# Optimization experiments

Hardware: AMD Instinct MI355X
Metric: run time of the kernel (lower is better)

The kernel has to match this reference:

```python
import jax, jax.numpy as jnp
import numpy as np

MARGIN = 1.0
EPS = 1e-6  # torch.nn.PairwiseDistance default eps (added to the difference vector)


def setup_inputs() -> dict:
    key = jax.random.key(0)
    k1, k2 = jax.random.split(key)
    B, D = 8192, 256
    out = jax.random.normal(k1, (B, D), dtype=jnp.float32)
    label = jax.random.randint(k2, (B,), 0, 2, dtype=jnp.int64)
    return {"out": out, "label": label}


def reference(out, label):
    B, D = out.shape
    # PairwiseDistance: dist_ij = || out_i - out_j + eps ||_2
    # Expand: sum_k (d_k + eps)^2 = ||d||^2 + 2*eps*sum_k d_k + D*eps^2
    sq_norm = jnp.sum(out * out, axis=-1)                       # [B]
    gram = out @ out.T                                          # [B, B]
    sq = sq_norm[:, None] + sq_norm[None, :] - 2.0 * gram       # ||out_i - out_j||^2
    row_sum = jnp.sum(out, axis=-1)                             # [B]
    sq_eps = sq + 2.0 * EPS * (row_sum[:, None] - row_sum[None, :]) + D * EPS * EPS
    dist = jnp.sqrt(jnp.maximum(sq_eps, 1e-12))                 # [B, B]

    same = label[:, None] == label[None, :]                     # [B, B] bool
    pos = dist * dist
    neg = jnp.square(jnp.maximum(MARGIN - dist, 0.0))
    per_pair = jnp.where(same, pos, neg)

    # only i < j pairs (strict upper triangle)
    tri = jnp.triu(jnp.ones((B, B), dtype=out.dtype), k=1)
    loss = jnp.sum(per_pair * tri)
    cnt = B * (B - 1) // 2
    return loss / (cnt + 1e-6)
```

## Files before the change

kernel.cpp:

```cpp
#include <hip/hip_runtime.h>
#include <hip/hip_fp8.h>

#define B_ 8192
#define D_ 256
#define KS_ 64
#define EPS_ 1e-6f
#define MARGIN_ 1.0f
#define NT_ 64
#define NTILES_ (NT_ * (NT_ + 1) / 2)
#define CEPS_ ((float)D_ * EPS_ * EPS_)
#define SCREEN_ 17.0f

typedef float floatx4 __attribute__((ext_vector_type(4)));

#define XBF_BYTES (B_ * D_ * 2)
#define OFF_P    0
#define OFF_Q    8192
#define OFF_S0   16384
#define OFF_S1   16640
#define OFF_N0   16896
#define OFF_N1   16897
#define OFF_C0   16898
#define OFF_ACC  16899
#define OFF_CNT  16900

__device__ __forceinline__ int trif(int t) { return (t * (129 - t)) / 2; }
__device__ __forceinline__ int decode_ti(int t) {
    int ti = (int)((129.0f - sqrtf(fmaxf(16641.0f - 8.0f * (float)t, 0.0f))) * 0.5f);
    ti = max(0, min(63, ti));
    while (trif(ti + 1) <= t) ++ti;
    while (trif(ti) > t) --ti;
    return ti;
}

__device__ __noinline__ float exact_hinge(const float* __restrict__ x, int gi, int gj,
                                          const int* __restrict__ label) {
    if (label[gi] == label[gj]) return 0.0f;
    const float* xi = x + (size_t)gi * D_;
    const float* xj = x + (size_t)gj * D_;
    float sq = 0.0f;
    for (int k = 0; k < D_; ++k) {
        const float df = xi[k] - xj[k] + EPS_;
        sq += df * df;
    }
    if (sq < 1.0f) {
        const float d = sqrtf(fmaxf(sq, 1e-12f));
        const float h = MARGIN_ - d;
        return h * h;
    }
    return 0.0f;
}

__global__ __launch_bounds__(256) void prep_kernel(
    const float* __restrict__ x, const int* __restrict__ label,
    unsigned char* __restrict__ xqT, float* __restrict__ fws) {
    float* pS = fws + OFF_P;   float* qS = fws + OFF_Q;

    __shared__ int lab_s[32];
    __shared__ float spn[32];
    __shared__ float colbuf0[4][256], colbuf1[4][256];

    const int blk = blockIdx.x;
    const int r0 = blk * 32;
    const int tid = threadIdx.x, w = tid >> 6, lane = tid & 63;

    if (blk == 0 && tid == 0) *(unsigned int*)(fws + OFF_CNT) = 0u;

    if (tid < 32) lab_s[tid] = label[r0 + tid];
    __syncthreads();

    floatx4 t0 = (floatx4)0.0f, t1 = (floatx4)0.0f;
    #pragma unroll
    for (int i = 0; i < 8; ++i) {
        const int rloc = w * 8 + i;
        const int row = r0 + rloc;
        const floatx4 v = *(const floatx4*)(x + (size_t)row * D_ + lane * 4);
        float sq = v[0]*v[0] + v[1]*v[1] + v[2]*v[2] + v[3]*v[3];
        float rs = v[0] + v[1] + v[2] + v[3];
        #pragma unroll
        for (int off = 8; off; off >>= 1) {
            sq += __shfl_down(sq, off);
            rs += __shfl_down(rs, off);
        }
        const float sqS = sq, rsS = rs;
        sq += __shfl_down(sq, 16); rs += __shfl_down(rs, 16);
        sq += __shfl_down(sq, 32); rs += __shfl_down(rs, 32);
        if (lane == 0) {
            pS[row] = sqS + 2.0f * EPS_ * rsS;
            qS[row] = sqS - 2.0f * EPS_ * rsS;
            spn[rloc] = sq;
        }
        if (lab_s[rloc]) t1 += v; else t0 += v;
        if (lane < 16) {
            __hip_fp8_e4m3 c0(v[0]), c1(v[1]), c2(v[2]), c3(v[3]);
            const unsigned int u = (unsigned int)c0.__x | ((unsigned int)c1.__x << 8)
                                 | ((unsigned int)c2.__x << 16) | ((unsigned int)c3.__x << 24);
            const int R = row >> 4, r = row & 15;
            const int ks = lane >> 3, quad = (lane >> 1) & 3, b = (lane & 1) * 4;
            *(unsigned int*)(xqT + (((R * 2 + ks) << 9) | (quad << 7) | (r << 3) | b)) = u;
        }
    }
    *(floatx4*)&colbuf0[w][lane * 4] = t0;
    *(floatx4*)&colbuf1[w][lane * 4] = t1;
    __syncthreads();

    atomicAdd(fws + OFF_S0 + tid,
              colbuf0[0][tid] + colbuf0[1][tid] + colbuf0[2][tid] + colbuf0[3][tid]);
    atomicAdd(fws + OFF_S1 + tid,
              colbuf1[0][tid] + colbuf1[1][tid] + colbuf1[2][tid] + colbuf1[3][tid]);

    if (tid < 32) {
        const float n = spn[tid];
        const int lb = lab_s[tid];
        float n0 = lb ? 0.0f : n, n1 = lb ? n : 0.0f;
        float c0 = lb ? 0.0f : 1.0f;
        #pragma unroll
        for (int off = 16; off; off >>= 1) {
            n0 += __shfl_down(n0, off);
            n1 += __shfl_down(n1, off);
            c0 += __shfl_down(c0, off);
        }
        if (tid == 0) {
            atomicAdd(fws + OFF_N0, n0);
            atomicAdd(fws + OFF_N1, n1);
            atomicAdd(fws + OFF_C0, c0);
        }
    }
}

__global__ __launch_bounds__(256, 3) void detect_kernel(
    const unsigned char* __restrict__ xqT, const float* __restrict__ x,
    const int* __restrict__ label, float* __restrict__ fws,
    float* __restrict__ out) {
    const float* pS = fws + OFF_P;  const float* qS = fws + OFF_Q;
    float* acc = fws + OFF_ACC;

    __shared__ int is_last;
    __shared__ float red[4];

    const int ti = decode_ti(blockIdx.x);
    const int tj = ti + (blockIdx.x - trif(ti));
    const int i0 = ti * 128, j0 = tj * 128;

    const int tid = threadIdx.x, wave = tid >> 6, lane = tid & 63;
    const int quad = lane >> 4, r = lane & 15;
    const int wm = wave >> 1, wn = wave & 1;

    const int Ri = (i0 >> 4) + wm * 4;
    const int Rj = (j0 >> 4) + wn * 4;
    const int lo = (quad << 7) | (r << 3);
    long av[8], bv[8];
    #pragma unroll
    for (int mt = 0; mt < 4; ++mt)
        #pragma unroll
        for (int ks = 0; ks < 2; ++ks) {
            av[mt * 2 + ks] = *(const long*)(xqT + ((((Ri + mt) * 2 + ks) << 9) | lo));
            bv[mt * 2 + ks] = *(const long*)(xqT + ((((Rj + mt) * 2 + ks) << 9) | lo));
        }

    floatx4 accv[16];
    #pragma unroll
    for (int t = 0; t < 16; ++t) accv[t] = (floatx4)0.0f;

    #pragma unroll
    for (int ks = 0; ks < 2; ++ks)
        #pragma unroll
        for (int mt = 0; mt < 4; ++mt)
            #pragma unroll
            for (int nt = 0; nt < 4; ++nt)
                accv[mt * 4 + nt] = __builtin_amdgcn_mfma_f32_16x16x32_fp8_fp8(
                    av[mt * 2 + ks], bv[nt * 2 + ks], accv[mt * 4 + nt], 0, 0, 0);

    float s = 0.0f;
    if (ti != tj) {
        float m = -1e30f;
        #pragma unroll
        for (int t = 0; t < 16; ++t)
            m = fmaxf(m, fmaxf(fmaxf(accv[t][0], accv[t][1]), fmaxf(accv[t][2], accv[t][3])));
        float pv = pS[i0 + wm * 64 + lane];
        float qv = qS[j0 + wn * 64 + lane];
        #pragma unroll
        for (int off = 32; off; off >>= 1) {
            pv = fminf(pv, __shfl_down(pv, off));
            qv = fminf(qv, __shfl_down(qv, off));
        }
        const float pmn = __shfl(pv, 0), qmn = __shfl(qv, 0);
        if (__any(2.0f * m > pmn + qmn - SCREEN_)) {
            float psr[16], qsr[4];
            #pragma unroll
            for (int mt = 0; mt < 4; ++mt)
                #pragma unroll
                for (int reg = 0; reg < 4; ++reg)
                    psr[mt * 4 + reg] = pS[i0 + wm * 64 + mt * 16 + quad * 4 + reg];
            #pragma unroll
            for (int nt = 0; nt < 4; ++nt)
                qsr[nt] = qS[j0 + wn * 64 + nt * 16 + r];
            #pragma unroll
            for (int mt = 0; mt < 4; ++mt)
                #pragma unroll
                for (int nt = 0; nt < 4; ++nt)
                    #pragma unroll
                    for (int reg = 0; reg < 4; ++reg) {
                        const float sq8 = psr[mt * 4 + reg] + qsr[nt]
                                        - 2.0f * accv[mt * 4 + nt][reg];
                        if (sq8 < SCREEN_) {
                            const int gi = i0 + wm * 64 + mt * 16 + quad * 4 + reg;
                            const int gj = j0 + wn * 64 + nt * 16 + r;
                            s += exact_hinge(x, gi, gj, label);
                        }
                    }
        }
    } else {
        float psr[16], qsr[4];
        #pragma unroll
        for (int mt = 0; mt < 4; ++mt)
            #pragma unroll
            for (int reg = 0; reg < 4; ++reg)
                psr[mt * 4 + reg] = pS[i0 + wm * 64 + mt * 16 + quad * 4 + reg];
        #pragma unroll
        for (int nt = 0; nt < 4; ++nt)
            qsr[nt] = qS[j0 + wn * 64 + nt * 16 + r];
        #pragma unroll
        for (int mt = 0; mt < 4; ++mt)
            #pragma unroll
            for (int nt = 0; nt < 4; ++nt)
                #pragma unroll
                for (int reg = 0; reg < 4; ++reg) {
                    const int il = wm * 64 + mt * 16 + quad * 4 + reg;
                    const int jl = wn * 64 + nt * 16 + r;
                    if (il < jl) {
                        const float sq8 = psr[mt * 4 + reg] + qsr[nt]
                                        - 2.0f * accv[mt * 4 + nt][reg];
                        if (sq8 < SCREEN_)
                            s += exact_hinge(x, i0 + il, j0 + jl, label);
                    }
                }
    }
    #pragma unroll
    for (int off = 32; off; off >>= 1) s += __shfl_down(s, off);
    if (lane == 0 && s != 0.0f) atomicAdd(acc, s);

    asm volatile("s_waitcnt vmcnt(0)" ::: "memory");
    __syncthreads();
    if (tid == 0) {
        const unsigned int old = atomicAdd((unsigned int*)(fws + OFF_CNT), 1u);
        is_last = (old == (unsigned int)(NTILES_ - 1));
    }
    __syncthreads();
    if (!is_last) return;

    const float a = fws[OFF_S0 + tid], b = fws[OFF_S1 + tid];
    float v = a * a + b * b;
    #pragma unroll
    for (int off = 32; off; off >>= 1) v += __shfl_down(v, off);
    if (lane == 0) red[wave] = v;
    __syncthreads();

    if (tid == 0) {
        const double Tsq = (double)red[0] + (double)red[1] + (double)red[2] + (double)red[3];
        const double N0 = fws[OFF_N0], N1 = fws[OFF_N1];
        const double C0r = fws[OFF_C0];
        const double C0 = (double)(long long)(C0r + 0.5);
        const double C1 = (double)B_ - C0;
        const double same = C0 * N0 + C1 * N1 - Tsq
                          + 0.5 * (C0 * (C0 - 1.0) + C1 * (C1 - 1.0)) * (double)CEPS_;
        const float hinge = atomicAdd(acc, 0.0f);
        const double total = same + (double)hinge;
        const double cnt = (double)B_ * (double)(B_ - 1) / 2.0 + 1e-6;
        out[0] = (float)(total / cnt);
    }
}

extern "C" void kernel_launch(void* const* d_in, const int* in_sizes, int n_in,
                              void* d_out, int out_size, void* d_ws, size_t ws_size,
                              hipStream_t stream) {
    const float* x = (const float*)d_in[0];
    const int* label = (const int*)d_in[1];
    float* out = (float*)d_out;

    char* ws = (char*)d_ws;
    unsigned char* xqT = (unsigned char*)ws;
    float* fws = (float*)(ws + XBF_BYTES);

    prep_kernel<<<B_ / 32, 256, 0, stream>>>(x, label, xqT, fws);
    detect_kernel<<<NTILES_, 256, 0, stream>>>(xqT, x, label, fws, out);
}
```

Baseline: 100.4 us.

## Process four column tiles per detect block and widen prep blocks

Each detect block now walks a chunk of up to four column tiles for one row tile. It reuses the A-fragment registers and the row min-norm reduction across the chunk, and the grid shrinks from 2080 to 544 blocks through a new block-to-tile decode. The prep kernel uses 1024-thread blocks with 2 rows per wave, and its column-sum reduction is widened to match. The intent is to cut per-block launch, decode and A-load overhead and shorten the tail. In exchange, each block runs its chunk serially, which lowers parallelism and may leave some CUs idle.

```diff
diff --git a/kernel.cpp b/kernel.cpp
--- a/kernel.cpp
+++ b/kernel.cpp
@@ -7,7 +7,8 @@
 #define EPS_ 1e-6f
 #define MARGIN_ 1.0f
 #define NT_ 64
-#define NTILES_ (NT_ * (NT_ + 1) / 2)
+#define CHUNK_ 4
+#define NBDET_ 544
 #define CEPS_ ((float)D_ * EPS_ * EPS_)
 #define SCREEN_ 17.0f
 
@@ -24,15 +25,6 @@
 #define OFF_ACC  16899
 #define OFF_CNT  16900
 
-__device__ __forceinline__ int trif(int t) { return (t * (129 - t)) / 2; }
-__device__ __forceinline__ int decode_ti(int t) {
-    int ti = (int)((129.0f - sqrtf(fmaxf(16641.0f - 8.0f * (float)t, 0.0f))) * 0.5f);
-    ti = max(0, min(63, ti));
-    while (trif(ti + 1) <= t) ++ti;
-    while (trif(ti) > t) --ti;
-    return ti;
-}
-
 __device__ __noinline__ float exact_hinge(const float* __restrict__ x, int gi, int gj,
                                           const int* __restrict__ label) {
     if (label[gi] == label[gj]) return 0.0f;
@@ -51,14 +43,14 @@
     return 0.0f;
 }
 
-__global__ __launch_bounds__(256) void prep_kernel(
+__global__ __launch_bounds__(1024) void prep_kernel(
     const float* __restrict__ x, const int* __restrict__ label,
     unsigned char* __restrict__ xqT, float* __restrict__ fws) {
     float* pS = fws + OFF_P;   float* qS = fws + OFF_Q;
 
     __shared__ int lab_s[32];
     __shared__ float spn[32];
-    __shared__ float colbuf0[4][256], colbuf1[4][256];
+    __shared__ float colbuf0[16][256], colbuf1[16][256];
 
     const int blk = blockIdx.x;
     const int r0 = blk * 32;
@@ -71,8 +63,8 @@
 
     floatx4 t0 = (floatx4)0.0f, t1 = (floatx4)0.0f;
     #pragma unroll
-    for (int i = 0; i < 8; ++i) {
-        const int rloc = w * 8 + i;
+    for (int i = 0; i < 2; ++i) {
+        const int rloc = w * 2 + i;
         const int row = r0 + rloc;
         const floatx4 v = *(const floatx4*)(x + (size_t)row * D_ + lane * 4);
         float sq = v[0]*v[0] + v[1]*v[1] + v[2]*v[2] + v[3]*v[3];
@@ -104,10 +96,13 @@
     *(floatx4*)&colbuf1[w][lane * 4] = t1;
     __syncthreads();
 
-    atomicAdd(fws + OFF_S0 + tid,
-              colbuf0[0][tid] + colbuf0[1][tid] + colbuf0[2][tid] + colbuf0[3][tid]);
-    atomicAdd(fws + OFF_S1 + tid,
-              colbuf1[0][tid] + colbuf1[1][tid] + colbuf1[2][tid] + colbuf1[3][tid]);
+    if (tid < 256) {
+        float a0 = 0.0f, a1 = 0.0f;
+        #pragma unroll
+        for (int k = 0; k < 16; ++k) { a0 += colbuf0[k][tid]; a1 += colbuf1[k][tid]; }
+        atomicAdd(fws + OFF_S0 + tid, a0);
+        atomicAdd(fws + OFF_S1 + tid, a1);
+    }
 
     if (tid < 32) {
         const float n = spn[tid];
@@ -138,54 +133,106 @@
     __shared__ int is_last;
     __shared__ float red[4];
 
-    const int ti = decode_ti(blockIdx.x);
-    const int tj = ti + (blockIdx.x - trif(ti));
-    const int i0 = ti * 128, j0 = tj * 128;
-
+    const int b = blockIdx.x;
+    int g = (int)((33.0f - sqrtf(fmaxf(1089.0f - 2.0f * (float)b, 0.0f))) * 0.5f);
+    g = max(0, min(15, g));
+    while (66 * (g + 1) - 2 * (g + 1) * (g + 1) <= b) ++g;
+    while (66 * g - 2 * g * g > b) --g;
+    const int rem = b - (66 * g - 2 * g * g);
+    const int nc = 16 - g;
+    const int q = rem / nc;
+    const int ti = 4 * g + q;
+    const int c = rem - q * nc;
+    const int tj0 = ti + 4 * c;
+
+    const int i0 = ti * 128;
     const int tid = threadIdx.x, wave = tid >> 6, lane = tid & 63;
     const int quad = lane >> 4, r = lane & 15;
     const int wm = wave >> 1, wn = wave & 1;
 
     const int Ri = (i0 >> 4) + wm * 4;
-    const int Rj = (j0 >> 4) + wn * 4;
     const int lo = (quad << 7) | (r << 3);
-    long av[8], bv[8];
+    long av[8];
     #pragma unroll
     for (int mt = 0; mt < 4; ++mt)
         #pragma unroll
-        for (int ks = 0; ks < 2; ++ks) {
+        for (int ks = 0; ks < 2; ++ks)
             av[mt * 2 + ks] = *(const long*)(xqT + ((((Ri + mt) * 2 + ks) << 9) | lo));
-            bv[mt * 2 + ks] = *(const long*)(xqT + ((((Rj + mt) * 2 + ks) << 9) | lo));
-        }
-
-    floatx4 accv[16];
-    #pragma unroll
-    for (int t = 0; t < 16; ++t) accv[t] = (floatx4)0.0f;
-
-    #pragma unroll
-    for (int ks = 0; ks < 2; ++ks)
+
+    float pv = pS[i0 + wm * 64 + lane];
+    #pragma unroll
+    for (int off = 32; off; off >>= 1) pv = fminf(pv, __shfl_down(pv, off));
+    const float pmn = __shfl(pv, 0);
+
+    float qvt[CHUNK_];
+    #pragma unroll
+    for (int t = 0; t < CHUNK_; ++t) {
+        const int tj = tj0 + t;
+        qvt[t] = (tj < NT_) ? qS[tj * 128 + wn * 64 + lane] : 0.0f;
+    }
+
+    float s = 0.0f;
+    for (int t = 0; t < CHUNK_; ++t) {
+        const int tj = tj0 + t;
+        if (tj >= NT_) break;
+        const int j0 = tj * 128;
+        const int Rj = (j0 >> 4) + wn * 4;
+
+        long bv[8];
         #pragma unroll
         for (int mt = 0; mt < 4; ++mt)
             #pragma unroll
-            for (int nt = 0; nt < 4; ++nt)
-                accv[mt * 4 + nt] = __builtin_amdgcn_mfma_f32_16x16x32_fp8_fp8(
-                    av[mt * 2 + ks], bv[nt * 2 + ks], accv[mt * 4 + nt], 0, 0, 0);
-
-    float s = 0.0f;
-    if (ti != tj) {
-        float m = -1e30f;
-        #pragma unroll
-        for (int t = 0; t < 16; ++t)
-            m = fmaxf(m, fmaxf(fmaxf(accv[t][0], accv[t][1]), fmaxf(accv[t][2], accv[t][3])));
-        float pv = pS[i0 + wm * 64 + lane];
-        float qv = qS[j0 + wn * 64 + lane];
-        #pragma unroll
-        for (int off = 32; off; off >>= 1) {
-            pv = fminf(pv, __shfl_down(pv, off));
-            qv = fminf(qv, __shfl_down(qv, off));
-        }
-        const float pmn = __shfl(pv, 0), qmn = __shfl(qv, 0);
-        if (__any(2.0f * m > pmn + qmn - SCREEN_)) {
+            for (int ks = 0; ks < 2; ++ks)
+                bv[mt * 2 + ks] = *(const long*)(xqT + ((((Rj + mt) * 2 + ks) << 9) | lo));
+
+        floatx4 accv[16];
+        #pragma unroll
+        for (int u = 0; u < 16; ++u) accv[u] = (floatx4)0.0f;
+
+        #pragma unroll
+        for (int ks = 0; ks < 2; ++ks)
+            #pragma unroll
+            for (int mt = 0; mt < 4; ++mt)
+                #pragma unroll
+                for (int nt = 0; nt < 4; ++nt)
+                    accv[mt * 4 + nt] = __builtin_amdgcn_mfma_f32_16x16x32_fp8_fp8(
+                        av[mt * 2 + ks], bv[nt * 2 + ks], accv[mt * 4 + nt], 0, 0, 0);
+
+        if (ti != tj) {
+            float m = -1e30f;
+            #pragma unroll
+            for (int u = 0; u < 16; ++u)
+                m = fmaxf(m, fmaxf(fmaxf(accv[u][0], accv[u][1]), fmaxf(accv[u][2], accv[u][3])));
+            float qv = qvt[t];
+            #pragma unroll
+            for (int off = 32; off; off >>= 1) qv = fminf(qv, __shfl_down(qv, off));
+            const float qmn = __shfl(qv, 0);
+            if (__any(2.0f * m > pmn + qmn - SCREEN_)) {
+                float psr[16], qsr[4];
+                #pragma unroll
+                for (int mt = 0; mt < 4; ++mt)
+                    #pragma unroll
+                    for (int reg = 0; reg < 4; ++reg)
+                        psr[mt * 4 + reg] = pS[i0 + wm * 64 + mt * 16 + quad * 4 + reg];
+                #pragma unroll
+                for (int nt = 0; nt < 4; ++nt)
+                    qsr[nt] = qS[j0 + wn * 64 + nt * 16 + r];
+                #pragma unroll
+                for (int mt = 0; mt < 4; ++mt)
+                    #pragma unroll
+                    for (int nt = 0; nt < 4; ++nt)
+                        #pragma unroll
+                        for (int reg = 0; reg < 4; ++reg) {
+                            const float sq8 = psr[mt * 4 + reg] + qsr[nt]
+                                            - 2.0f * accv[mt * 4 + nt][reg];
+                            if (sq8 < SCREEN_) {
+                                const int gi = i0 + wm * 64 + mt * 16 + quad * 4 + reg;
+                                const int gj = j0 + wn * 64 + nt * 16 + r;
+                                s += exact_hinge(x, gi, gj, label);
+                            }
+                        }
+            }
+        } else {
             float psr[16], qsr[4];
             #pragma unroll
             for (int mt = 0; mt < 4; ++mt)
@@ -201,56 +248,35 @@
                 for (int nt = 0; nt < 4; ++nt)
                     #pragma unroll
                     for (int reg = 0; reg < 4; ++reg) {
-                        const float sq8 = psr[mt * 4 + reg] + qsr[nt]
-                                        - 2.0f * accv[mt * 4 + nt][reg];
-                        if (sq8 < SCREEN_) {
-                            const int gi = i0 + wm * 64 + mt * 16 + quad * 4 + reg;
-                            const int gj = j0 + wn * 64 + nt * 16 + r;
-                            s += exact_hinge(x, gi, gj, label);
+                        const int il = wm * 64 + mt * 16 + quad * 4 + reg;
+                        const int jl = wn * 64 + nt * 16 + r;
+                        if (il < jl) {
+                            const float sq8 = psr[mt * 4 + reg] + qsr[nt]
+                                            - 2.0f * accv[mt * 4 + nt][reg];
+                            if (sq8 < SCREEN_)
+                                s += exact_hinge(x, i0 + il, j0 + jl, label);
                         }
                     }
         }
-    } else {
-        float psr[16], qsr[4];
-        #pragma unroll
-        for (int mt = 0; mt < 4; ++mt)
-            #pragma unroll
-            for (int reg = 0; reg < 4; ++reg)
-                psr[mt * 4 + reg] = pS[i0 + wm * 64 + mt * 16 + quad * 4 + reg];
-        #pragma unroll
-        for (int nt = 0; nt < 4; ++nt)
-            qsr[nt] = qS[j0 + wn * 64 + nt * 16 + r];
-        #pragma unroll
-        for (int mt = 0; mt < 4; ++mt)
-            #pragma unroll
-            for (int nt = 0; nt < 4; ++nt)
-                #pragma unroll
-                for (int reg = 0; reg < 4; ++reg) {
-                    const int il = wm * 64 + mt * 16 + quad * 4 + reg;
-                    const int jl = wn * 64 + nt * 16 + r;
-                    if (il < jl) {
-                        const float sq8 = psr[mt * 4 + reg] + qsr[nt]
-                                        - 2.0f * accv[mt * 4 + nt][reg];
-                        if (sq8 < SCREEN_)
-                            s += exact_hinge(x, i0 + il, j0 + jl, label);
-                    }
-                }
     }
     #pragma unroll
     for (int off = 32; off; off >>= 1) s += __shfl_down(s, off);
-    if (lane == 0 && s != 0.0f) atomicAdd(acc, s);
+    if (lane == 0 && s != 0.0f) {
+        const float old = atomicAdd(acc, s);
+        asm volatile("" :: "v"(old));
+    }
 
     asm volatile("s_waitcnt vmcnt(0)" ::: "memory");
     __syncthreads();
     if (tid == 0) {
         const unsigned int old = atomicAdd((unsigned int*)(fws + OFF_CNT), 1u);
-        is_last = (old == (unsigned int)(NTILES_ - 1));
+        is_last = (old == (unsigned int)(NBDET_ - 1));
     }
     __syncthreads();
     if (!is_last) return;
 
-    const float a = fws[OFF_S0 + tid], b = fws[OFF_S1 + tid];
-    float v = a * a + b * b;
+    const float a = fws[OFF_S0 + tid], bb = fws[OFF_S1 + tid];
+    float v = a * a + bb * bb;
     #pragma unroll
     for (int off = 32; off; off >>= 1) v += __shfl_down(v, off);
     if (lane == 0) red[wave] = v;
@@ -282,6 +308,6 @@
     unsigned char* xqT = (unsigned char*)ws;
     float* fws = (float*)(ws + XBF_BYTES);
 
-    prep_kernel<<<B_ / 32, 256, 0, stream>>>(x, label, xqT, fws);
-    detect_kernel<<<NTILES_, 256, 0, stream>>>(xqT, x, label, fws, out);
+    prep_kernel<<<B_ / 32, 1024, 0, stream>>>(x, label, xqT, fws);
+    detect_kernel<<<NBDET_, 256, 0, stream>>>(xqT, x, label, fws, out);
 }
```

After: 96.76 us. -3.6%, faster.
